# Optimization experiments

Hardware: AMD Instinct MI355X
Metric: run time of the kernel (lower is better)

## Reference

```python
import jax, jax.numpy as jnp
import numpy as np

BLOCK = 32          # MXFP block size (OCP microscaling)
EMAX_FP4 = 2.0      # max exponent of FP4 E2M1 (max value 6.0 = 1.5 * 2^2)
FP4_MAX = 6.0       # saturation value of E2M1
E8M0_MIN, E8M0_MAX = -127.0, 127.0


def _quant_dequant_mxfp(t, block_dim):
    """Fake-quantize tensor t to MXFP4 (E2M1 elements, shared E8M0 scale per
    block of 32 along block_dim), then dequantize back to float."""
    t = jnp.moveaxis(t, block_dim, -1)
    shape = t.shape
    nb = shape[-1] // BLOCK
    tb = t.reshape(shape[:-1] + (nb, BLOCK))

    # shared power-of-two scale from block absmax: scale = 2^(floor(log2 amax) - emax)
    amax = jnp.max(jnp.abs(tb), axis=-1, keepdims=True)
    safe_amax = jnp.where(amax > 0, amax, 1.0)
    shared_exp = jnp.floor(jnp.log2(safe_amax)) - EMAX_FP4
    scale = jnp.exp2(jnp.clip(shared_exp, E8M0_MIN, E8M0_MAX))

    v = tb / scale
    sign = jnp.sign(v)
    a = jnp.clip(jnp.abs(v), 0.0, FP4_MAX)  # saturate to E2M1 max
    # E2M1 quantization step: 0.5 for |v|<2 (incl. subnormals), 1 for [2,4), 2 for [4,6]
    e = jnp.clip(jnp.floor(jnp.log2(jnp.maximum(a, 2.0 ** -10))), 0.0, EMAX_FP4)
    step = jnp.exp2(e - 1.0)
    q = jnp.round(a / step) * step

    deq = (sign * q * scale).reshape(shape)
    return jnp.moveaxis(deq, -1, block_dim)


def setup_inputs() -> dict:
    key = jax.random.key(0)
    kx, kw, kb = jax.random.split(key, 3)
    x = jax.random.normal(kx, (64, 4096), dtype=jnp.float32)
    weight = jax.random.normal(kw, (11008, 4096), dtype=jnp.float32) * 0.02
    bias = jax.random.normal(kb, (11008,), dtype=jnp.float32) * 0.02
    return {"x": x, "weight": weight, "bias": bias}


def reference(x, weight, bias):
    # layer_type = 'XqWqBq': MXFP4 quant-dequant on x (last dim), w (in_features
    # dim, block_dim=1) and b (dim 0), fused with the linear GEMM.
    x_dq = _quant_dequant_mxfp(x, block_dim=-1)        # [T, Din]
    w_dq = _quant_dequant_mxfp(weight, block_dim=1)    # [Dout, Din]
    b_dq = _quant_dequant_mxfp(bias, block_dim=0)      # [Dout]
    return jnp.einsum('ti,oi->to', x_dq, w_dq) + b_dq  # [T, Dout]
```

## Files before the change

### kernel.cpp

```cpp
#include <hip/hip_runtime.h>
#include <hip/hip_bf16.h>

#define DIN    4096
#define DOUT   11008
#define TM     64
#define KSPLIT 4
#define KCHUNK (DIN / KSPLIT)
#define NCHUNKS (DOUT / 16)

typedef __attribute__((ext_vector_type(8))) short  bf16x8;
typedef __attribute__((ext_vector_type(4))) float  f32x4;

__device__ inline void mx_block_scale(float amax, float& scale, float& inv_scale) {
    float safe = amax > 0.0f ? amax : 1.0f;
    int e  = (int)((__float_as_uint(safe) >> 23) & 255) - 127;
    int se = e - 2;
    if (se < -127) se = -127;
    scale     = ldexpf(1.0f, se);
    inv_scale = ldexpf(1.0f, -se);
}

__device__ inline float mx_qd(float v, float scale, float inv_scale) {
    float a = fabsf(v) * inv_scale;
    a = fminf(a, 6.0f);
    float step  = (a < 2.0f) ? 0.5f : (a < 4.0f) ? 1.0f : 2.0f;
    float rstep = (a < 2.0f) ? 2.0f : (a < 4.0f) ? 1.0f : 0.5f;
    float q = rintf(a * rstep) * step;
    return copysignf(q * scale, v);
}

__device__ inline short bf16_trunc(float f) {
    return (short)(__float_as_uint(f) >> 16);
}

__device__ inline float blk_absmax8(const float4& a, const float4& b) {
    return fmaxf(fmaxf(fmaxf(fabsf(a.x), fabsf(a.y)), fmaxf(fabsf(a.z), fabsf(a.w))),
                 fmaxf(fmaxf(fabsf(b.x), fabsf(b.y)), fmaxf(fabsf(b.z), fabsf(b.w))));
}

__global__ __launch_bounds__(256) void quant_x_kernel(const float* __restrict__ x,
                                                      unsigned short* __restrict__ x_dq) {
    int gid = blockIdx.x * 256 + threadIdx.x;
    const float4 v = *(const float4*)(x + (size_t)gid * 4);
    float am = fmaxf(fmaxf(fabsf(v.x), fabsf(v.y)), fmaxf(fabsf(v.z), fabsf(v.w)));
    am = fmaxf(am, __shfl_xor(am, 1));
    am = fmaxf(am, __shfl_xor(am, 2));
    am = fmaxf(am, __shfl_xor(am, 4));
    float scale, inv;
    mx_block_scale(am, scale, inv);
    ushort4 q;
    q.x = (unsigned short)bf16_trunc(mx_qd(v.x, scale, inv));
    q.y = (unsigned short)bf16_trunc(mx_qd(v.y, scale, inv));
    q.z = (unsigned short)bf16_trunc(mx_qd(v.z, scale, inv));
    q.w = (unsigned short)bf16_trunc(mx_qd(v.w, scale, inv));
    *(ushort4*)(x_dq + (size_t)gid * 4) = q;
}

__global__ __launch_bounds__(256) void gemm_kernel(const unsigned short* __restrict__ x_dq,
                                                   const float* __restrict__ wgt,
                                                   float* __restrict__ partial) {
    const int lane  = threadIdx.x & 63;
    const int wid   = threadIdx.x >> 6;
    const int w     = blockIdx.x * 4 + wid;
    const int nch   = w % NCHUNKS;
    const int split = w / NCHUNKS;
    const int nlo   = lane & 15;
    const int kq    = lane >> 4;
    const int kbase = split * KCHUNK + kq * 8;

    const float*          wp = wgt  + (size_t)(nch * 16 + nlo) * DIN + kbase;
    const unsigned short* xp = x_dq + (size_t)nlo * DIN + kbase;

    f32x4 acc0 = {0.f,0.f,0.f,0.f};
    f32x4 acc1 = {0.f,0.f,0.f,0.f};
    f32x4 acc2 = {0.f,0.f,0.f,0.f};
    f32x4 acc3 = {0.f,0.f,0.f,0.f};

    float4 wa0 = *(const float4*)(wp);
    float4 wa1 = *(const float4*)(wp + 4);
    float4 wb0 = *(const float4*)(wp + 32);
    float4 wb1 = *(const float4*)(wp + 36);
    float am = blk_absmax8(wa0, wa1);
    am = fmaxf(am, __shfl_xor(am, 16));
    am = fmaxf(am, __shfl_xor(am, 32));
    float scale, inv;
    mx_block_scale(am, scale, inv);

    #pragma unroll 4
    for (int kk = 0; kk < KCHUNK; kk += 32) {
        const int kpre = (kk + 64 < KCHUNK) ? kk + 64 : KCHUNK - 32;
        float4 wc0 = *(const float4*)(wp + kpre);
        float4 wc1 = *(const float4*)(wp + kpre + 4);

        bf16x8 a0 = *(const bf16x8*)(xp + kk);
        bf16x8 a1 = *(const bf16x8*)(xp + 16 * DIN + kk);
        bf16x8 a2 = *(const bf16x8*)(xp + 32 * DIN + kk);
        bf16x8 a3 = *(const bf16x8*)(xp + 48 * DIN + kk);

        bf16x8 bf;
        bf[0] = bf16_trunc(mx_qd(wa0.x, scale, inv));
        bf[1] = bf16_trunc(mx_qd(wa0.y, scale, inv));
        bf[2] = bf16_trunc(mx_qd(wa0.z, scale, inv));
        bf[3] = bf16_trunc(mx_qd(wa0.w, scale, inv));
        bf[4] = bf16_trunc(mx_qd(wa1.x, scale, inv));
        bf[5] = bf16_trunc(mx_qd(wa1.y, scale, inv));
        bf[6] = bf16_trunc(mx_qd(wa1.z, scale, inv));
        bf[7] = bf16_trunc(mx_qd(wa1.w, scale, inv));

        acc0 = __builtin_amdgcn_mfma_f32_16x16x32_bf16(a0, bf, acc0, 0, 0, 0);
        acc1 = __builtin_amdgcn_mfma_f32_16x16x32_bf16(a1, bf, acc1, 0, 0, 0);
        acc2 = __builtin_amdgcn_mfma_f32_16x16x32_bf16(a2, bf, acc2, 0, 0, 0);
        acc3 = __builtin_amdgcn_mfma_f32_16x16x32_bf16(a3, bf, acc3, 0, 0, 0);

        float amn = blk_absmax8(wb0, wb1);
        amn = fmaxf(amn, __shfl_xor(amn, 16));
        amn = fmaxf(amn, __shfl_xor(amn, 32));
        mx_block_scale(amn, scale, inv);

        wa0 = wb0; wa1 = wb1;
        wb0 = wc0; wb1 = wc1;
    }

    float* pp = partial + (size_t)split * (TM * DOUT) + (size_t)(nch * 16 + nlo);
    const int mrow = kq * 4;
    #pragma unroll
    for (int r = 0; r < 4; ++r) {
        pp[(size_t)(mrow + r) * DOUT]      = acc0[r];
        pp[(size_t)(16 + mrow + r) * DOUT] = acc1[r];
        pp[(size_t)(32 + mrow + r) * DOUT] = acc2[r];
        pp[(size_t)(48 + mrow + r) * DOUT] = acc3[r];
    }
}

__global__ __launch_bounds__(256) void reduce_bias_kernel(const float* __restrict__ partial,
                                                          const float* __restrict__ bias,
                                                          float* __restrict__ out) {
    int gid = blockIdx.x * 256 + threadIdx.x;
    float s = 0.f;
    #pragma unroll
    for (int i = 0; i < KSPLIT; ++i)
        s += partial[(size_t)i * (TM * DOUT) + gid];
    int n = gid % DOUT;
    float v = bias[n];
    float am = fabsf(v);
    am = fmaxf(am, __shfl_xor(am, 1));
    am = fmaxf(am, __shfl_xor(am, 2));
    am = fmaxf(am, __shfl_xor(am, 4));
    am = fmaxf(am, __shfl_xor(am, 8));
    am = fmaxf(am, __shfl_xor(am, 16));
    float scale, inv;
    mx_block_scale(am, scale, inv);
    out[gid] = s + mx_qd(v, scale, inv);
}

extern "C" void kernel_launch(void* const* d_in, const int* in_sizes, int n_in,
                              void* d_out, int out_size, void* d_ws, size_t ws_size,
                              hipStream_t stream) {
    const float* x    = (const float*)d_in[0];
    const float* wgt  = (const float*)d_in[1];
    const float* bias = (const float*)d_in[2];
    float* out = (float*)d_out;

    unsigned short* x_dq    = (unsigned short*)d_ws;
    float*          partial = (float*)((char*)d_ws + 512 * 1024);

    quant_x_kernel<<<256, 256, 0, stream>>>(x, x_dq);
    gemm_kernel<<<NCHUNKS * KSPLIT / 4, 256, 0, stream>>>(x_dq, wgt, partial);
    reduce_bias_kernel<<<TM * DOUT / 256, 256, 0, stream>>>(partial, bias, out);
}
```

Before: 281.0 us.

## Fuse split-K reduction and bias quantization into GEMM via shared memory

Each block now owns one 16-column output chunk, and its four waves each handle a quarter of K. The partial sums are reduced in LDS and the quantized bias is added in-kernel, which removes the partial buffer round-trip through global memory and the separate reduce kernel launch. The FP4 step and reciprocal-step selection is also replaced with exponent bit arithmetic instead of compare chains. The cost is an extra __syncthreads, LDS use per block, and a different mapping of blocks to waves.

```diff
diff --git a/kernel.cpp b/kernel.cpp
--- a/kernel.cpp
+++ b/kernel.cpp
@@ -23,8 +23,10 @@
 __device__ inline float mx_qd(float v, float scale, float inv_scale) {
     float a = fabsf(v) * inv_scale;
     a = fminf(a, 6.0f);
-    float step  = (a < 2.0f) ? 0.5f : (a < 4.0f) ? 1.0f : 2.0f;
-    float rstep = (a < 2.0f) ? 2.0f : (a < 4.0f) ? 1.0f : 0.5f;
+    unsigned ebc = __float_as_uint(a) & 0x7f800000u;
+    ebc = ebc < 0x3f800000u ? 0x3f800000u : ebc;
+    float step  = __uint_as_float(ebc - 0x00800000u);
+    float rstep = __uint_as_float(0x7f800000u - ebc);
     float q = rintf(a * rstep) * step;
     return copysignf(q * scale, v);
 }
@@ -56,17 +58,32 @@
     *(ushort4*)(x_dq + (size_t)gid * 4) = q;
 }
 
-__global__ __launch_bounds__(256) void gemm_kernel(const unsigned short* __restrict__ x_dq,
-                                                   const float* __restrict__ wgt,
-                                                   float* __restrict__ partial) {
+__global__ __launch_bounds__(256) void gemm_fused_kernel(const unsigned short* __restrict__ x_dq,
+                                                         const float* __restrict__ wgt,
+                                                         const float* __restrict__ bias,
+                                                         float* __restrict__ out) {
     const int lane  = threadIdx.x & 63;
     const int wid   = threadIdx.x >> 6;
-    const int w     = blockIdx.x * 4 + wid;
-    const int nch   = w % NCHUNKS;
-    const int split = w / NCHUNKS;
+    const int nch   = blockIdx.x;
     const int nlo   = lane & 15;
     const int kq    = lane >> 4;
-    const int kbase = split * KCHUNK + kq * 8;
+    const int kbase = wid * KCHUNK + kq * 8;
+
+    __shared__ float red[KSPLIT][TM][20];
+    __shared__ float bq[32];
+
+    if (threadIdx.x < 32) {
+        float v = bias[(nch >> 1) * 32 + threadIdx.x];
+        float am = fabsf(v);
+        am = fmaxf(am, __shfl_xor(am, 1));
+        am = fmaxf(am, __shfl_xor(am, 2));
+        am = fmaxf(am, __shfl_xor(am, 4));
+        am = fmaxf(am, __shfl_xor(am, 8));
+        am = fmaxf(am, __shfl_xor(am, 16));
+        float scale, inv;
+        mx_block_scale(am, scale, inv);
+        bq[threadIdx.x] = mx_qd(v, scale, inv);
+    }
 
     const float*          wp = wgt  + (size_t)(nch * 16 + nlo) * DIN + kbase;
     const unsigned short* xp = x_dq + (size_t)nlo * DIN + kbase;
@@ -121,36 +138,26 @@
         wb0 = wc0; wb1 = wc1;
     }
 
-    float* pp = partial + (size_t)split * (TM * DOUT) + (size_t)(nch * 16 + nlo);
     const int mrow = kq * 4;
     #pragma unroll
     for (int r = 0; r < 4; ++r) {
-        pp[(size_t)(mrow + r) * DOUT]      = acc0[r];
-        pp[(size_t)(16 + mrow + r) * DOUT] = acc1[r];
-        pp[(size_t)(32 + mrow + r) * DOUT] = acc2[r];
-        pp[(size_t)(48 + mrow + r) * DOUT] = acc3[r];
+        red[wid][mrow + r][nlo]      = acc0[r];
+        red[wid][16 + mrow + r][nlo] = acc1[r];
+        red[wid][32 + mrow + r][nlo] = acc2[r];
+        red[wid][48 + mrow + r][nlo] = acc3[r];
     }
-}
+    __syncthreads();
 
-__global__ __launch_bounds__(256) void reduce_bias_kernel(const float* __restrict__ partial,
-                                                          const float* __restrict__ bias,
-                                                          float* __restrict__ out) {
-    int gid = blockIdx.x * 256 + threadIdx.x;
-    float s = 0.f;
+    const int col  = threadIdx.x & 15;
+    const int row0 = threadIdx.x >> 4;
+    const float b  = bq[((nch & 1) << 4) + col];
+    float* op = out + (size_t)nch * 16 + col;
     #pragma unroll
-    for (int i = 0; i < KSPLIT; ++i)
-        s += partial[(size_t)i * (TM * DOUT) + gid];
-    int n = gid % DOUT;
-    float v = bias[n];
-    float am = fabsf(v);
-    am = fmaxf(am, __shfl_xor(am, 1));
-    am = fmaxf(am, __shfl_xor(am, 2));
-    am = fmaxf(am, __shfl_xor(am, 4));
-    am = fmaxf(am, __shfl_xor(am, 8));
-    am = fmaxf(am, __shfl_xor(am, 16));
-    float scale, inv;
-    mx_block_scale(am, scale, inv);
-    out[gid] = s + mx_qd(v, scale, inv);
+    for (int t = 0; t < 4; ++t) {
+        const int row = row0 + 16 * t;
+        float s = ((red[0][row][col] + red[1][row][col]) + red[2][row][col]) + red[3][row][col];
+        op[(size_t)row * DOUT] = s + b;
+    }
 }
 
 extern "C" void kernel_launch(void* const* d_in, const int* in_sizes, int n_in,
@@ -161,10 +168,8 @@
     const float* bias = (const float*)d_in[2];
     float* out = (float*)d_out;
 
-    unsigned short* x_dq    = (unsigned short*)d_ws;
-    float*          partial = (float*)((char*)d_ws + 512 * 1024);
+    unsigned short* x_dq = (unsigned short*)d_ws;
 
     quant_x_kernel<<<256, 256, 0, stream>>>(x, x_dq);
-    gemm_kernel<<<NCHUNKS * KSPLIT / 4, 256, 0, stream>>>(x_dq, wgt, partial);
-    reduce_bias_kernel<<<TM * DOUT / 256, 256, 0, stream>>>(partial, bias, out);
+    gemm_fused_kernel<<<NCHUNKS, 256, 0, stream>>>(x_dq, wgt, bias, out);
 }
```

After: 279.6 us, median of 2. No clear change (-0.5%).
